# Kernel tuning notes

Hardware: AMD Instinct MI355X
Metric: run time of the kernel (lower is better)

Reference implementation:

```python
import jax, jax.numpy as jnp
import numpy as np

N_POINTS = 65536
N0 = 65536
N_NEIGH = 32
K = 15
IN_F = 64
OUT_F = 128
RADIUS = 0.1
KP_EXTENT = 1.2 * RADIUS / 5.0  # config.KP_extent * radius / density_parameter
BN_EPS = 1e-6
NEG_SLOPE = 0.1


def setup_inputs() -> dict:
    key = jax.random.key(0)
    ks = jax.random.split(key, 8)
    cloud_scale = 0.05  # neighbor offsets ~ KP_EXTENT so influences are nonzero
    query_points = jax.random.uniform(ks[0], (N_POINTS, 3), jnp.float32) * cloud_scale
    support_points = jax.random.uniform(ks[1], (N0, 3), jnp.float32) * cloud_scale
    neighbors_indices = jax.random.randint(ks[2], (N_POINTS, N_NEIGH), 0, N0, jnp.int32)
    features = jax.random.normal(ks[3], (N0, IN_F), jnp.float32)
    # fixed kernel point dispositions, scaled to the kernel extent
    kernel_points = jax.random.normal(ks[4], (K, 3), jnp.float32) * (KP_EXTENT / 1.5)
    W = jax.random.normal(ks[5], (K, IN_F, OUT_F), jnp.float32) * np.sqrt(2.0 / OUT_F)
    gamma = jnp.ones((OUT_F,), jnp.float32)
    beta = jnp.zeros((OUT_F,), jnp.float32)
    return {
        "query_points": query_points,
        "support_points": support_points,
        "neighbors_indices": neighbors_indices,
        "features": features,
        "kernel_points": kernel_points,
        "W": W,
        "gamma": gamma,
        "beta": beta,
    }


def reference(query_points, support_points, neighbors_indices, features,
              kernel_points, W, gamma, beta):
    # --- KPConv: gather neighbors, kernel-point linear influence, sum aggregation ---
    # shadow point far away with zero features (handles out-of-range indices in original)
    sp = jnp.concatenate([support_points,
                          jnp.full((1, 3), 1e6, support_points.dtype)], axis=0)
    feat = jnp.concatenate([features,
                            jnp.zeros((1, features.shape[1]), features.dtype)], axis=0)
    neighbors = sp[neighbors_indices]                      # [n, m, 3]
    diffs = neighbors - query_points[:, None, :]           # [n, m, 3]
    # squared distances to each kernel point: [n, m, K]
    sq = jnp.sum((diffs[:, :, None, :] - kernel_points[None, None, :, :]) ** 2, axis=-1)
    # linear influence, 'sum' aggregation mode
    all_w = jnp.maximum(0.0, 1.0 - jnp.sqrt(sq) / KP_EXTENT)  # [n, m, K]
    all_w = jnp.transpose(all_w, (0, 2, 1))                   # [n, K, m]
    neighb_x = feat[neighbors_indices]                        # [n, m, in]
    weighted = jnp.einsum('nkm,nmi->nki', all_w, neighb_x)    # [n, K, in]
    x = jnp.einsum('nki,kio->no', weighted, W)                # [n, out]
    # --- BatchNorm1d (training-mode batch stats) + LeakyReLU(0.1) ---
    mean = jnp.mean(x, axis=0)
    var = jnp.var(x, axis=0)
    x = (x - mean) * jax.lax.rsqrt(var + BN_EPS) * gamma + beta
    return jnp.where(x >= 0, x, NEG_SLOPE * x)
```

## Files before the change

kernel.cpp:

```cpp
#include <hip/hip_runtime.h>

#define NPTS  65536
#define NNEI  32
#define NKP   15
#define INF   64
#define OUTF  128
#define PPB   16
#define KT_N  32
#define NSETS 64
#define INV_KPE 41.666666666666664f
#define BN_EPS 1e-6f
#define NEG_SLOPE 0.1f

typedef __attribute__((ext_vector_type(8))) short  bf16x8;
typedef __attribute__((ext_vector_type(4))) float  f32x4;

__device__ unsigned short g_Wp[KT_N * 8 * 64 * 8];
__device__ unsigned short g_featb[NPTS * INF];
__device__ float g_part[NSETS][2 * OUTF];
__device__ float g_scale[OUTF], g_shift[OUTF];

__device__ __forceinline__ unsigned short f2b(float f) {
    union { float f; unsigned int i; } v; v.f = f;
    unsigned int x = v.i;
    return (unsigned short)((x + 0x7fffu + ((x >> 16) & 1u)) >> 16);
}
__device__ __forceinline__ unsigned int pk2(float a, float b) {
    return (unsigned int)f2b(a) | ((unsigned int)f2b(b) << 16);
}
__device__ __forceinline__ bf16x8 mk8(unsigned int a, unsigned int b,
                                      unsigned int c, unsigned int d) {
    unsigned int t[4] = {a, b, c, d};
    bf16x8 r; __builtin_memcpy(&r, t, 16); return r;
}

__global__ __launch_bounds__(256) void pack_inputs(const float* __restrict__ W,
                                                   const float* __restrict__ feat) {
    const int b = blockIdx.x, t = threadIdx.x;
    if (b < NSETS) g_part[b][t] = 0.0f;
    if (b < 512) {
        int id = b * 256 + t;
        int j  = id & 7;
        int ln = (id >> 3) & 63;
        int nt = (id >> 9) & 7;
        int kt = id >> 12;
        int i  = kt * 32 + ((ln >> 4) * 8) + j;
        int kp = i & 15;
        int ch = i >> 4;
        int o  = nt * 16 + (ln & 15);
        g_Wp[id] = (kp < NKP) ? f2b(W[(kp * 64 + ch) * 128 + o]) : (unsigned short)0;
    } else {
        int id = (b - 512) * 256 + t;
        const float4 v = ((const float4*)feat)[id];
        uint2 r; r.x = pk2(v.x, v.y); r.y = pk2(v.z, v.w);
        ((uint2*)g_featb)[id] = r;
    }
}

__global__ __launch_bounds__(256, 4) void kpconv_fused(
        const float* __restrict__ qp,
        const float* __restrict__ sp,
        const int*   __restrict__ nbr,
        const float* __restrict__ kp,
        float*       __restrict__ out)
{
    __shared__ __align__(16) unsigned short wlds[128 * PPB * 8];
    __shared__ float dbuf[4][128][3];
    __shared__ int   ibuf[4][128];

    const int tid  = threadIdx.x;
    const int lane = tid & 63;
    const int wv   = tid >> 6;
    const int q    = lane >> 4;
    const int c16  = lane & 15;
    const int gp0  = blockIdx.x * PPB + wv * 4;

#pragma unroll
    for (int rep = 0; rep < 2; ++rep) {
        const int pt  = rep * 2 + (lane >> 5);
        const int m   = lane & 31;
        const int gpt = gp0 + pt;
        const int idx = nbr[gpt * NNEI + m];
        ibuf[wv][pt * 32 + m] = idx;
        dbuf[wv][pt * 32 + m][0] = sp[idx * 3 + 0] - qp[gpt * 3 + 0];
        dbuf[wv][pt * 32 + m][1] = sp[idx * 3 + 1] - qp[gpt * 3 + 1];
        dbuf[wv][pt * 32 + m][2] = sp[idx * 3 + 2] - qp[gpt * 3 + 2];
    }
    float kx, ky, kz;
    if (c16 < NKP) { kx = kp[c16 * 3]; ky = kp[c16 * 3 + 1]; kz = kp[c16 * 3 + 2]; }
    else           { kx = ky = kz = 1.0e6f; }

    uint2 dcur[8], dnxt[8];
#pragma unroll
    for (int j = 0; j < 8; ++j) {
        const int idx = ibuf[wv][q * 8 + j];
        dcur[j] = *(const uint2*)&g_featb[idx * INF + c16 * 4];
    }

#pragma unroll
    for (int pt = 0; pt < 4; ++pt) {
        const int pl = wv * 4 + pt;

        if (pt < 3) {
#pragma unroll
            for (int j = 0; j < 8; ++j) {
                const int idx = ibuf[wv][(pt + 1) * 32 + q * 8 + j];
                dnxt[j] = *(const uint2*)&g_featb[idx * INF + c16 * 4];
            }
        }

        float w8[8];
#pragma unroll
        for (int j = 0; j < 8; ++j) {
            const int m = pt * 32 + q * 8 + j;
            const float ex = dbuf[wv][m][0] - kx;
            const float ey = dbuf[wv][m][1] - ky;
            const float ez = dbuf[wv][m][2] - kz;
            const float s  = ex * ex + ey * ey + ez * ez;
            const float w  = 1.0f - __builtin_amdgcn_sqrtf(s) * INV_KPE;
            w8[j] = (w > 0.0f) ? w : 0.0f;
        }
        const bf16x8 af = mk8(pk2(w8[0], w8[1]), pk2(w8[2], w8[3]),
                              pk2(w8[4], w8[5]), pk2(w8[6], w8[7]));

        f32x4 acc[4] = {{0.f,0.f,0.f,0.f},{0.f,0.f,0.f,0.f},
                        {0.f,0.f,0.f,0.f},{0.f,0.f,0.f,0.f}};
#pragma unroll
        for (int nt = 0; nt < 4; ++nt) {
            unsigned int dw[4];
#pragma unroll
            for (int p = 0; p < 4; ++p) {
                const unsigned int lo = (nt < 2) ? dcur[2 * p].x     : dcur[2 * p].y;
                const unsigned int hi = (nt < 2) ? dcur[2 * p + 1].x : dcur[2 * p + 1].y;
                dw[p] = (nt & 1) ? ((lo >> 16) | (hi & 0xffff0000u))
                                 : ((lo & 0xffffu) | (hi << 16));
            }
            acc[nt] = __builtin_amdgcn_mfma_f32_16x16x32_bf16(
                af, mk8(dw[0], dw[1], dw[2], dw[3]), acc[nt], 0, 0, 0);
        }

#pragma unroll
        for (int nt = 0; nt < 4; ++nt) {
            uint2 pv;
            pv.x = pk2(acc[nt][0], acc[nt][1]);
            pv.y = pk2(acc[nt][2], acc[nt][3]);
            const int ibase = (c16 * 4 + nt) * 16 + q * 4;
            const int g   = ibase >> 3;
            const int off = ibase & 7;
            const int plx = pl ^ ((g >> 3) & 7);
            *(uint2*)&wlds[(g * PPB + plx) * 8 + off] = pv;
        }

#pragma unroll
        for (int j = 0; j < 8; ++j) dcur[j] = dnxt[j];
    }
    __syncthreads();

    const int nt0 = wv * 2;
    f32x4 a00 = {0.f,0.f,0.f,0.f}, a01 = {0.f,0.f,0.f,0.f};

    for (int kt = 0; kt < KT_N; ++kt) {
        const int g   = kt * 4 + q;
        const int plx = c16 ^ ((g >> 3) & 7);
        const bf16x8 fa  = *(const bf16x8*)&wlds[(g * PPB + plx) * 8];
        const bf16x8 fb0 = *(const bf16x8*)&g_Wp[((kt * 8 + nt0) * 64 + lane) * 8];
        const bf16x8 fb1 = *(const bf16x8*)&g_Wp[((kt * 8 + nt0 + 1) * 64 + lane) * 8];
        a00 = __builtin_amdgcn_mfma_f32_16x16x32_bf16(fa, fb0, a00, 0, 0, 0);
        a01 = __builtin_amdgcn_mfma_f32_16x16x32_bf16(fa, fb1, a01, 0, 0, 0);
    }

    const int rb = blockIdx.x * PPB + q * 4;
    const int c0 = nt0 * 16 + c16;
    float s0 = 0.f, q0 = 0.f, s1 = 0.f, q1 = 0.f;
#pragma unroll
    for (int r = 0; r < 4; ++r) {
        const float v0 = a00[r], v1 = a01[r];
        out[(rb + r) * OUTF + c0]      = v0;
        out[(rb + r) * OUTF + c0 + 16] = v1;
        s0 += v0; q0 += v0 * v0;
        s1 += v1; q1 += v1 * v1;
    }
    s0 += __shfl_xor(s0, 16); s0 += __shfl_xor(s0, 32);
    q0 += __shfl_xor(q0, 16); q0 += __shfl_xor(q0, 32);
    s1 += __shfl_xor(s1, 16); s1 += __shfl_xor(s1, 32);
    q1 += __shfl_xor(q1, 16); q1 += __shfl_xor(q1, 32);
    const int set = blockIdx.x & (NSETS - 1);
    if (lane < 16) {
        atomicAdd(&g_part[set][nt0 * 16 + lane],            s0);
        atomicAdd(&g_part[set][OUTF + nt0 * 16 + lane],     q0);
        atomicAdd(&g_part[set][nt0 * 16 + 16 + lane],       s1);
        atomicAdd(&g_part[set][OUTF + nt0 * 16 + 16 + lane], q1);
    }
}

__global__ void bn_scaleshift(const float* __restrict__ gamma,
                              const float* __restrict__ beta) {
    const int o = threadIdx.x;
    float s = 0.f, qq = 0.f;
    for (int i = 0; i < NSETS; ++i) { s += g_part[i][o]; qq += g_part[i][OUTF + o]; }
    const float inv_n = 1.0f / (float)NPTS;
    const float mean  = s * inv_n;
    const float var   = qq * inv_n - mean * mean;
    const float sc    = gamma[o] * rsqrtf(var + BN_EPS);
    g_scale[o] = sc;
    g_shift[o] = beta[o] - mean * sc;
}

__global__ __launch_bounds__(256) void bn_norm(float* __restrict__ x) {
    const int id   = blockIdx.x * 256 + threadIdx.x;
    const int base = id * 4;
    const int o0   = base & 127;
    float4 v = *(const float4*)&x[base];
    const float4 sc = *(const float4*)&g_scale[o0];
    const float4 sf = *(const float4*)&g_shift[o0];
    float y0 = v.x * sc.x + sf.x;
    float y1 = v.y * sc.y + sf.y;
    float y2 = v.z * sc.z + sf.z;
    float y3 = v.w * sc.w + sf.w;
    y0 = (y0 >= 0.f) ? y0 : NEG_SLOPE * y0;
    y1 = (y1 >= 0.f) ? y1 : NEG_SLOPE * y1;
    y2 = (y2 >= 0.f) ? y2 : NEG_SLOPE * y2;
    y3 = (y3 >= 0.f) ? y3 : NEG_SLOPE * y3;
    float4 res = {y0, y1, y2, y3};
    *(float4*)&x[base] = res;
}

extern "C" void kernel_launch(void* const* d_in, const int* in_sizes, int n_in,
                              void* d_out, int out_size, void* d_ws, size_t ws_size,
                              hipStream_t stream) {
    const float* qp    = (const float*)d_in[0];
    const float* sp    = (const float*)d_in[1];
    const int*   nbr   = (const int*)d_in[2];
    const float* kp    = (const float*)d_in[4];
    const float* W     = (const float*)d_in[5];
    const float* gamma = (const float*)d_in[6];
    const float* beta  = (const float*)d_in[7];
    const float* feat  = (const float*)d_in[3];
    float* out = (float*)d_out;

    pack_inputs<<<512 + 4096, 256, 0, stream>>>(W, feat);
    kpconv_fused<<<NPTS / PPB, 256, 0, stream>>>(qp, sp, nbr, kp, out);
    bn_scaleshift<<<1, 128, 0, stream>>>(gamma, beta);
    bn_norm<<<(NPTS * OUTF) / (256 * 4), 256, 0, stream>>>(out);
}
```

Baseline: 190.4 us.

## Store pre-BN activations as bf16, fuse BN stats into norm, batch gathers

The fused conv kernel now writes its pre-normalization output as bf16 to a scratch buffer instead of fp32 to the output, halving that intermediate traffic. The separate scale/shift kernel is folded into the normalization kernel: each block recomputes the per-channel stats into shared memory, and each thread processes 8 elements per iteration. All four points' neighbor feature gathers are issued up front rather than double-buffered, which raises register use. Rounding activations to bf16 before BN adds precision loss.

```diff
diff --git a/kernel.cpp b/kernel.cpp
--- a/kernel.cpp
+++ b/kernel.cpp
@@ -11,15 +11,19 @@
 #define INV_KPE 41.666666666666664f
 #define BN_EPS 1e-6f
 #define NEG_SLOPE 0.1f
+#define INV_N (1.0f / 65536.0f)
 
 typedef __attribute__((ext_vector_type(8))) short  bf16x8;
 typedef __attribute__((ext_vector_type(4))) float  f32x4;
 
 __device__ unsigned short g_Wp[KT_N * 8 * 64 * 8];
 __device__ unsigned short g_featb[NPTS * INF];
+__device__ __align__(16) unsigned short g_xb[NPTS * OUTF];
 __device__ float g_part[NSETS][2 * OUTF];
-__device__ float g_scale[OUTF], g_shift[OUTF];
-
+
+__device__ __forceinline__ float b2f(unsigned short u) {
+    union { unsigned int i; float f; } v; v.i = ((unsigned int)u) << 16; return v.f;
+}
 __device__ __forceinline__ unsigned short f2b(float f) {
     union { float f; unsigned int i; } v; v.f = f;
     unsigned int x = v.i;
@@ -61,8 +65,7 @@
         const float* __restrict__ qp,
         const float* __restrict__ sp,
         const int*   __restrict__ nbr,
-        const float* __restrict__ kp,
-        float*       __restrict__ out)
+        const float* __restrict__ kp)
 {
     __shared__ __align__(16) unsigned short wlds[128 * PPB * 8];
     __shared__ float dbuf[4][128][3];
@@ -90,24 +93,19 @@
     if (c16 < NKP) { kx = kp[c16 * 3]; ky = kp[c16 * 3 + 1]; kz = kp[c16 * 3 + 2]; }
     else           { kx = ky = kz = 1.0e6f; }
 
-    uint2 dcur[8], dnxt[8];
-#pragma unroll
-    for (int j = 0; j < 8; ++j) {
-        const int idx = ibuf[wv][q * 8 + j];
-        dcur[j] = *(const uint2*)&g_featb[idx * INF + c16 * 4];
+    uint2 d[4][8];
+#pragma unroll
+    for (int pt = 0; pt < 4; ++pt) {
+#pragma unroll
+        for (int j = 0; j < 8; ++j) {
+            const int idx = ibuf[wv][pt * 32 + q * 8 + j];
+            d[pt][j] = *(const uint2*)&g_featb[idx * INF + c16 * 4];
+        }
     }
 
 #pragma unroll
     for (int pt = 0; pt < 4; ++pt) {
         const int pl = wv * 4 + pt;
-
-        if (pt < 3) {
-#pragma unroll
-            for (int j = 0; j < 8; ++j) {
-                const int idx = ibuf[wv][(pt + 1) * 32 + q * 8 + j];
-                dnxt[j] = *(const uint2*)&g_featb[idx * INF + c16 * 4];
-            }
-        }
 
         float w8[8];
 #pragma unroll
@@ -130,8 +128,8 @@
             unsigned int dw[4];
 #pragma unroll
             for (int p = 0; p < 4; ++p) {
-                const unsigned int lo = (nt < 2) ? dcur[2 * p].x     : dcur[2 * p].y;
-                const unsigned int hi = (nt < 2) ? dcur[2 * p + 1].x : dcur[2 * p + 1].y;
+                const unsigned int lo = (nt < 2) ? d[pt][2 * p].x     : d[pt][2 * p].y;
+                const unsigned int hi = (nt < 2) ? d[pt][2 * p + 1].x : d[pt][2 * p + 1].y;
                 dw[p] = (nt & 1) ? ((lo >> 16) | (hi & 0xffff0000u))
                                  : ((lo & 0xffffu) | (hi << 16));
             }
@@ -150,9 +148,6 @@
             const int plx = pl ^ ((g >> 3) & 7);
             *(uint2*)&wlds[(g * PPB + plx) * 8 + off] = pv;
         }
-
-#pragma unroll
-        for (int j = 0; j < 8; ++j) dcur[j] = dnxt[j];
     }
     __syncthreads();
 
@@ -175,8 +170,8 @@
 #pragma unroll
     for (int r = 0; r < 4; ++r) {
         const float v0 = a00[r], v1 = a01[r];
-        out[(rb + r) * OUTF + c0]      = v0;
-        out[(rb + r) * OUTF + c0 + 16] = v1;
+        g_xb[(rb + r) * OUTF + c0]      = f2b(v0);
+        g_xb[(rb + r) * OUTF + c0 + 16] = f2b(v1);
         s0 += v0; q0 += v0 * v0;
         s1 += v1; q1 += v1 * v1;
     }
@@ -186,43 +181,52 @@
     q1 += __shfl_xor(q1, 16); q1 += __shfl_xor(q1, 32);
     const int set = blockIdx.x & (NSETS - 1);
     if (lane < 16) {
-        atomicAdd(&g_part[set][nt0 * 16 + lane],            s0);
-        atomicAdd(&g_part[set][OUTF + nt0 * 16 + lane],     q0);
-        atomicAdd(&g_part[set][nt0 * 16 + 16 + lane],       s1);
+        atomicAdd(&g_part[set][nt0 * 16 + lane],             s0);
+        atomicAdd(&g_part[set][OUTF + nt0 * 16 + lane],      q0);
+        atomicAdd(&g_part[set][nt0 * 16 + 16 + lane],        s1);
         atomicAdd(&g_part[set][OUTF + nt0 * 16 + 16 + lane], q1);
     }
 }
 
-__global__ void bn_scaleshift(const float* __restrict__ gamma,
-                              const float* __restrict__ beta) {
-    const int o = threadIdx.x;
-    float s = 0.f, qq = 0.f;
-    for (int i = 0; i < NSETS; ++i) { s += g_part[i][o]; qq += g_part[i][OUTF + o]; }
-    const float inv_n = 1.0f / (float)NPTS;
-    const float mean  = s * inv_n;
-    const float var   = qq * inv_n - mean * mean;
-    const float sc    = gamma[o] * rsqrtf(var + BN_EPS);
-    g_scale[o] = sc;
-    g_shift[o] = beta[o] - mean * sc;
-}
-
-__global__ __launch_bounds__(256) void bn_norm(float* __restrict__ x) {
-    const int id   = blockIdx.x * 256 + threadIdx.x;
-    const int base = id * 4;
-    const int o0   = base & 127;
-    float4 v = *(const float4*)&x[base];
-    const float4 sc = *(const float4*)&g_scale[o0];
-    const float4 sf = *(const float4*)&g_shift[o0];
-    float y0 = v.x * sc.x + sf.x;
-    float y1 = v.y * sc.y + sf.y;
-    float y2 = v.z * sc.z + sf.z;
-    float y3 = v.w * sc.w + sf.w;
-    y0 = (y0 >= 0.f) ? y0 : NEG_SLOPE * y0;
-    y1 = (y1 >= 0.f) ? y1 : NEG_SLOPE * y1;
-    y2 = (y2 >= 0.f) ? y2 : NEG_SLOPE * y2;
-    y3 = (y3 >= 0.f) ? y3 : NEG_SLOPE * y3;
-    float4 res = {y0, y1, y2, y3};
-    *(float4*)&x[base] = res;
+__global__ __launch_bounds__(256) void bn_norm(const float* __restrict__ gamma,
+                                               const float* __restrict__ beta,
+                                               float* __restrict__ out) {
+    __shared__ float ssc[OUTF], ssf[OUTF];
+    const int t = threadIdx.x;
+    if (t < OUTF) {
+        float s = 0.f, qq = 0.f;
+#pragma unroll 8
+        for (int i = 0; i < NSETS; ++i) { s += g_part[i][t]; qq += g_part[i][OUTF + t]; }
+        const float mean = s * INV_N;
+        const float var  = qq * INV_N - mean * mean;
+        const float sc   = gamma[t] * rsqrtf(var + BN_EPS);
+        ssc[t] = sc;
+        ssf[t] = beta[t] - mean * sc;
+    }
+    __syncthreads();
+
+#pragma unroll
+    for (int it = 0; it < 4; ++it) {
+        const int id   = (blockIdx.x * 4 + it) * 256 + t;
+        const int base = id * 8;
+        const int o0   = base & 127;
+        const uint4 v  = *(const uint4*)&g_xb[base];
+        const unsigned int wds[4] = {v.x, v.y, v.z, v.w};
+        float y[8];
+#pragma unroll
+        for (int p = 0; p < 4; ++p) {
+            const float x0 = b2f((unsigned short)(wds[p] & 0xffffu));
+            const float x1 = b2f((unsigned short)(wds[p] >> 16));
+            float y0 = x0 * ssc[o0 + 2 * p]     + ssf[o0 + 2 * p];
+            float y1 = x1 * ssc[o0 + 2 * p + 1] + ssf[o0 + 2 * p + 1];
+            y[2 * p]     = (y0 >= 0.f) ? y0 : NEG_SLOPE * y0;
+            y[2 * p + 1] = (y1 >= 0.f) ? y1 : NEG_SLOPE * y1;
+        }
+        float4 r0 = {y[0], y[1], y[2], y[3]};
+        float4 r1 = {y[4], y[5], y[6], y[7]};
+        *(float4*)&out[base]     = r0;
+        *(float4*)&out[base + 4] = r1;
+    }
 }
 
 extern "C" void kernel_launch(void* const* d_in, const int* in_sizes, int n_in,
@@ -231,15 +235,14 @@
     const float* qp    = (const float*)d_in[0];
     const float* sp    = (const float*)d_in[1];
     const int*   nbr   = (const int*)d_in[2];
+    const float* feat  = (const float*)d_in[3];
     const float* kp    = (const float*)d_in[4];
     const float* W     = (const float*)d_in[5];
     const float* gamma = (const float*)d_in[6];
     const float* beta  = (const float*)d_in[7];
-    const float* feat  = (const float*)d_in[3];
     float* out = (float*)d_out;
 
     pack_inputs<<<512 + 4096, 256, 0, stream>>>(W, feat);
-    kpconv_fused<<<NPTS / PPB, 256, 0, stream>>>(qp, sp, nbr, kp, out);
-    bn_scaleshift<<<1, 128, 0, stream>>>(gamma, beta);
-    bn_norm<<<(NPTS * OUTF) / (256 * 4), 256, 0, stream>>>(out);
-}
+    kpconv_fused<<<NPTS / PPB, 256, 0, stream>>>(qp, sp, nbr, kp);
+    bn_norm<<<1024, 256, 0, stream>>>(gamma, beta, out);
+}
```

After: 190.4 us. About the same (+0.0%).
